# Kernel tuning notes

Measured on AMD Instinct MI355X. Metric: run time of the kernel, lower is better.

The kernel has to match this reference:

```python
import jax, jax.numpy as jnp
import numpy as np

P0 = 2   # tublet_size
P = 16   # patch_size
FC = 2   # flow channels (map_x, map_y)


def patchify(x, p0, p1, p2):
    # x: (B, C, T, H, W) -> (B, (T/p0)(H/p1)(W/p2), p0*p1*p2*C)
    B, C, T, H, W = x.shape
    x = x.reshape(B, C, T // p0, p0, H // p1, p1, W // p2, p2)
    x = x.transpose(0, 2, 4, 6, 3, 5, 7, 1)  # b t h w p0 p1 p2 c
    return x.reshape(B, (T // p0) * (H // p1) * (W // p2), p0 * p1 * p2 * C)


def unpatchify(x, p0, p1, p2, C, T, H, W):
    # x: (B, N, p0*p1*p2*C) -> (B, C, T, H, W)
    B = x.shape[0]
    x = x.reshape(B, T // p0, H // p1, W // p2, p0, p1, p2, C)
    x = x.transpose(0, 7, 1, 4, 2, 5, 3, 6)  # b c t p0 h p1 w p2
    return x.reshape(B, C, T, H, W)


def bilinear_warp(imgs, mx, my):
    # imgs: (B, C, T, H, W); mx, my: (B, T, H, W) absolute sample coords.
    # Equivalent of cv2.remap INTER_LINEAR with constant (zero) border.
    B, C, T, H, W = imgs.shape
    x0 = jnp.floor(mx)
    y0 = jnp.floor(my)
    wx = (mx - x0).reshape(B, 1, T, H * W)
    wy = (my - y0).reshape(B, 1, T, H * W)
    x0i = x0.astype(jnp.int32)
    y0i = y0.astype(jnp.int32)
    imgs_flat = imgs.reshape(B, C, T, H * W)

    def gather(yi, xi):
        yc = jnp.clip(yi, 0, H - 1)
        xc = jnp.clip(xi, 0, W - 1)
        idx = (yc * W + xc).reshape(B, 1, T, H * W)
        v = jnp.take_along_axis(imgs_flat, jnp.broadcast_to(idx, (B, C, T, H * W)), axis=-1)
        valid = ((yi >= 0) & (yi <= H - 1) & (xi >= 0) & (xi <= W - 1)).reshape(B, 1, T, H * W)
        return v * valid.astype(v.dtype)

    v00 = gather(y0i, x0i)
    v01 = gather(y0i, x0i + 1)
    v10 = gather(y0i + 1, x0i)
    v11 = gather(y0i + 1, x0i + 1)
    out = (v00 * (1 - wx) * (1 - wy) + v01 * wx * (1 - wy)
           + v10 * (1 - wx) * wy + v11 * wx * wy)
    return out.reshape(B, C, T, H, W)


def setup_inputs() -> dict:
    key = jax.random.key(0)
    k1, k2, k3 = jax.random.split(key, 3)
    B, C, T, H, W = 8, 3, 16, 224, 224
    N = (T // P0) * (H // P) * (W // P)         # 1568 tokens
    D = P0 * P * P * FC                         # 1024 per-token flow dim
    output = jax.random.normal(k1, (B, N, D), dtype=jnp.float32)
    raw_target = jax.random.normal(k2, (B, C, T, H, W), dtype=jnp.float32)
    mask = jax.random.randint(k3, (B, N), 0, 2) > 0
    return {"output": output, "raw_target": raw_target, "mask": mask}


def reference(output, raw_target, mask):
    B, C, T, H, W = raw_target.shape
    # tokens -> dense flow field (B, 2, T, H, W)
    flows = unpatchify(output, P0, P, P, FC, T, H, W)
    gx = jnp.arange(W, dtype=flows.dtype)               # (W,)
    gy = jnp.arange(H, dtype=flows.dtype)[:, None]      # (H, 1)
    mx = flows[:, 0] + gx                                # (B, T, H, W)
    my = flows[:, 1] + gy
    recons = bilinear_warp(raw_target, mx, my)           # (B, C, T, H, W)
    rec_p = patchify(recons, P0, P, P)                   # (B, N, p0*p1*p2*C)
    tgt_p = patchify(raw_target, P0, P, P)
    m = mask.astype(rec_p.dtype)[..., None]              # (B, N, 1)
    diff2 = (rec_p - tgt_p) ** 2 * m
    denom = jnp.maximum(m.sum(), 1.0) * rec_p.shape[-1]
    return diff2.sum() / denom
```

## Files before the change

### kernel.cpp

```cpp
#include <hip/hip_runtime.h>

#define Bd 8
#define Cd 3
#define Td 16
#define Hd 224
#define Wd 224
#define Nd 1568
#define HWd (Hd*Wd)
#define NPH 14
#define NPW 14
#define NT2 8
#define NSTRIP (Bd*NT2*NPH)
#define NUNIT (NSTRIP*2)
#define GRID_MAIN (NUNIT*3)
#define UPX (NUNIT/8)
#define HALO 2
#define SROWS (16 + 2*HALO)
#define LROW Wd
#define LDS_FLOATS (SROWS*LROW)
#define STG_GRAN (SROWS*56)
#define PATCH_ELEMS 1536.0

typedef const float __attribute__((address_space(1))) gfloat;
typedef float __attribute__((address_space(3))) sfloat;

__global__ __launch_bounds__(256, 8)
void flow_mse_strip(const float* __restrict__ outp,
                    const float* __restrict__ raw,
                    const int* __restrict__ mask,
                    float* __restrict__ partial,
                    int* __restrict__ scnt) {
    __shared__ float lds[LDS_FLOATS];
    __shared__ float sred[4];

    const int tid  = threadIdx.x;
    const int bid  = blockIdx.x;
    const int xcd  = bid & 7;
    const int slot = bid >> 3;
    const int c    = slot % 3;
    const int ul   = slot / 3;
    const int u    = xcd * UPX + ul;
    const int strip = u >> 1;
    const int i0    = u & 1;
    const int b     = strip / (NT2 * NPH);
    const int sr    = strip - b * (NT2 * NPH);
    const int t2    = sr / NPH;
    const int ph    = sr - t2 * NPH;
    const int t     = (t2 << 1) | i0;
    const int ybase = (ph << 4) - HALO;

    const float* plane = raw + ((size_t)(b * Cd + c) * Td + t) * HWd;
    #pragma unroll
    for (int it = 0; it < 5; ++it) {
        int v = tid + (it << 8);
        if (v < STG_GRAN) {
            int j    = v / 56;
            int col4 = v - j * 56;
            int yc   = min(max(ybase + j, 0), Hd - 1);
            const float* g = plane + yc * Wd + (col4 << 2);
            __builtin_amdgcn_global_load_lds((gfloat*)g, (sfloat*)(lds + (v << 2)),
                                             16, 0, 0);
        }
    }

    const int nbase = t2 * 196 + ph * NPW;
    const int lane  = tid & 63;
    bool mm = false;
    if (lane < NPW) mm = (mask[b * Nd + nbase + lane] != 0);
    const unsigned mw0   = (unsigned)(__ballot(mm) & 0x3FFFull);
    const int      tkcnt = __popc(mw0);

    __syncthreads();

    float acc = 0.f;
    const int py = tid >> 4, px = tid & 15;
    const int h  = (ph << 4) + py;
    const int bt = (py + HALO) * LROW;

    unsigned mw = mw0;
    while (mw) {
        const int pw = __ffs((int)mw) - 1;
        mw &= mw - 1;

        const float* fpf = outp + (((size_t)(b * Nd + nbase + pw)) << 10) + (i0 << 9);
        float2 f = ((const float2*)fpf)[tid];

        const int w = (pw << 4) + px;
        float mx = f.x + (float)w;
        float my = f.y + (float)h;
        float x0 = floorf(mx), y0 = floorf(my);
        float wx = mx - x0,    wy = my - y0;
        int x0i = (int)x0, y0i = (int)y0;
        int x1i = x0i + 1,  y1i = y0i + 1;

        bool vx0 = (x0i >= 0) && (x0i < Wd);
        bool vx1 = (x1i >= 0) && (x1i < Wd);
        bool vy0 = (y0i >= 0) && (y0i < Hd);
        bool vy1 = (y1i >= 0) && (y1i < Hd);

        float W00 = (1.f - wx) * (1.f - wy) * ((vx0 && vy0) ? 1.f : 0.f);
        float W01 = wx         * (1.f - wy) * ((vx1 && vy0) ? 1.f : 0.f);
        float W10 = (1.f - wx) * wy         * ((vx0 && vy1) ? 1.f : 0.f);
        float W11 = wx         * wy         * ((vx1 && vy1) ? 1.f : 0.f);

        int xc0 = min(max(x0i, 0), Wd - 1);
        int xc1 = min(max(x1i, 0), Wd - 1);
        int yc0 = min(max(y0i, 0), Hd - 1);
        int yc1 = min(max(y1i, 0), Hd - 1);
        int ly0 = yc0 - ybase, ly1 = yc1 - ybase;

        float tg = lds[bt + w];
        float rec;
        if ((ly0 >= 0) & (ly1 < SROWS)) {
            rec = lds[ly0 * LROW + xc0] * W00 + lds[ly0 * LROW + xc1] * W01
                + lds[ly1 * LROW + xc0] * W10 + lds[ly1 * LROW + xc1] * W11;
        } else {
            rec = plane[yc0 * Wd + xc0] * W00 + plane[yc0 * Wd + xc1] * W01
                + plane[yc1 * Wd + xc0] * W10 + plane[yc1 * Wd + xc1] * W11;
        }
        float d = rec - tg;
        acc += d * d;
    }

    for (int off = 32; off > 0; off >>= 1) acc += __shfl_down(acc, off, 64);
    if ((tid & 63) == 0) sred[tid >> 6] = acc;
    __syncthreads();
    if (tid == 0) {
        partial[bid] = sred[0] + sred[1] + sred[2] + sred[3];
        if (c == 0 && i0 == 0) scnt[strip] = tkcnt;
    }
}

__global__ void finalize_kernel(const float* __restrict__ partial,
                                const int* __restrict__ scnt,
                                float* __restrict__ out) {
    const int tid = threadIdx.x;
    double s = 0.0;
    for (int i = tid; i < GRID_MAIN; i += 256) s += (double)partial[i];
    int c = 0;
    for (int i = tid; i < NSTRIP; i += 256) c += scnt[i];
    for (int off = 32; off > 0; off >>= 1) {
        s += __shfl_down(s, off, 64);
        c += __shfl_down(c, off, 64);
    }
    __shared__ double sd[4];
    __shared__ int    sc[4];
    int lane = tid & 63, wid = tid >> 6;
    if (lane == 0) { sd[wid] = s; sc[wid] = c; }
    __syncthreads();
    if (tid == 0) {
        double st = sd[0] + sd[1] + sd[2] + sd[3];
        int    ct = sc[0] + sc[1] + sc[2] + sc[3];
        double denom = (double)(ct > 0 ? ct : 1) * PATCH_ELEMS;
        out[0] = (float)(st / denom);
    }
}

extern "C" void kernel_launch(void* const* d_in, const int* in_sizes, int n_in,
                              void* d_out, int out_size, void* d_ws, size_t ws_size,
                              hipStream_t stream) {
    const float* outp = (const float*)d_in[0];
    const float* raw  = (const float*)d_in[1];
    const int*   mask = (const int*)d_in[2];
    float* out = (float*)d_out;

    float* partial = (float*)d_ws;
    int*   scnt    = (int*)((char*)d_ws + GRID_MAIN * 4);

    flow_mse_strip<<<GRID_MAIN, 256, 0, stream>>>(outp, raw, mask, partial, scnt);
    finalize_kernel<<<1, 256, 0, stream>>>(partial, scnt, out);
}
```

Measured before the change: 160.3 us.

## Replace LDS strip staging with per-token direct global gather kernel

The kernel drops the per-strip LDS staging of image rows (with halo) and instead launches one block per token and frame, which exits early if the token is masked off. Each block gathers the bilinear taps and the target pixel straight from global memory for all three channels, so the flow is loaded once for all channels instead of once per channel block. The aim is to avoid staging rows that masked tokens never use and to drop the LDS fill and barrier. The cost is that neighbouring tokens no longer share staged data, so the design relies on the cache. The final kernel now counts the mask directly, and the grid grows to about 25k mostly short blocks.

```diff
diff --git a/kernel.cpp b/kernel.cpp
--- a/kernel.cpp
+++ b/kernel.cpp
@@ -7,138 +7,93 @@
 #define Wd 224
 #define Nd 1568
 #define HWd (Hd*Wd)
-#define NPH 14
-#define NPW 14
-#define NT2 8
-#define NSTRIP (Bd*NT2*NPH)
-#define NUNIT (NSTRIP*2)
-#define GRID_MAIN (NUNIT*3)
-#define UPX (NUNIT/8)
-#define HALO 2
-#define SROWS (16 + 2*HALO)
-#define LROW Wd
-#define LDS_FLOATS (SROWS*LROW)
-#define STG_GRAN (SROWS*56)
+#define NTOK (Bd*Nd)
+#define GRID_MAIN (NTOK*2)
 #define PATCH_ELEMS 1536.0
 
-typedef const float __attribute__((address_space(1))) gfloat;
-typedef float __attribute__((address_space(3))) sfloat;
+__global__ __launch_bounds__(256, 8)
+void flow_mse_gather(const float* __restrict__ outp,
+                     const float* __restrict__ raw,
+                     const int* __restrict__ mask,
+                     float* __restrict__ partial) {
+    const int tid = threadIdx.x;
+    const int bid = blockIdx.x;
+    const int ft  = bid >> 1;
+    const int i0  = bid & 1;
 
-__global__ __launch_bounds__(256, 8)
-void flow_mse_strip(const float* __restrict__ outp,
-                    const float* __restrict__ raw,
-                    const int* __restrict__ mask,
-                    float* __restrict__ partial,
-                    int* __restrict__ scnt) {
-    __shared__ float lds[LDS_FLOATS];
-    __shared__ float sred[4];
-
-    const int tid  = threadIdx.x;
-    const int bid  = blockIdx.x;
-    const int xcd  = bid & 7;
-    const int slot = bid >> 3;
-    const int c    = slot % 3;
-    const int ul   = slot / 3;
-    const int u    = xcd * UPX + ul;
-    const int strip = u >> 1;
-    const int i0    = u & 1;
-    const int b     = strip / (NT2 * NPH);
-    const int sr    = strip - b * (NT2 * NPH);
-    const int t2    = sr / NPH;
-    const int ph    = sr - t2 * NPH;
-    const int t     = (t2 << 1) | i0;
-    const int ybase = (ph << 4) - HALO;
-
-    const float* plane = raw + ((size_t)(b * Cd + c) * Td + t) * HWd;
-    #pragma unroll
-    for (int it = 0; it < 5; ++it) {
-        int v = tid + (it << 8);
-        if (v < STG_GRAN) {
-            int j    = v / 56;
-            int col4 = v - j * 56;
-            int yc   = min(max(ybase + j, 0), Hd - 1);
-            const float* g = plane + yc * Wd + (col4 << 2);
-            __builtin_amdgcn_global_load_lds((gfloat*)g, (sfloat*)(lds + (v << 2)),
-                                             16, 0, 0);
-        }
+    if (mask[ft] == 0) {
+        if (tid == 0) partial[bid] = 0.f;
+        return;
     }
 
-    const int nbase = t2 * 196 + ph * NPW;
-    const int lane  = tid & 63;
-    bool mm = false;
-    if (lane < NPW) mm = (mask[b * Nd + nbase + lane] != 0);
-    const unsigned mw0   = (unsigned)(__ballot(mm) & 0x3FFFull);
-    const int      tkcnt = __popc(mw0);
+    const int b  = ft / Nd;
+    const int n  = ft - b * Nd;
+    const int t2 = n / 196;
+    const int rm = n - t2 * 196;
+    const int ph = rm / 14;
+    const int pw = rm - ph * 14;
+    const int t  = (t2 << 1) | i0;
 
-    __syncthreads();
-
-    float acc = 0.f;
     const int py = tid >> 4, px = tid & 15;
     const int h  = (ph << 4) + py;
-    const int bt = (py + HALO) * LROW;
+    const int w  = (pw << 4) + px;
 
-    unsigned mw = mw0;
-    while (mw) {
-        const int pw = __ffs((int)mw) - 1;
-        mw &= mw - 1;
+    const float2 f = ((const float2*)(outp + ((size_t)ft << 10) + (i0 << 9)))[tid];
 
-        const float* fpf = outp + (((size_t)(b * Nd + nbase + pw)) << 10) + (i0 << 9);
-        float2 f = ((const float2*)fpf)[tid];
+    const float mx = f.x + (float)w;
+    const float my = f.y + (float)h;
+    const float x0 = floorf(mx), y0 = floorf(my);
+    const float wx = mx - x0,    wy = my - y0;
+    const int x0i = (int)x0, y0i = (int)y0;
+    const int x1i = x0i + 1,  y1i = y0i + 1;
 
-        const int w = (pw << 4) + px;
-        float mx = f.x + (float)w;
-        float my = f.y + (float)h;
-        float x0 = floorf(mx), y0 = floorf(my);
-        float wx = mx - x0,    wy = my - y0;
-        int x0i = (int)x0, y0i = (int)y0;
-        int x1i = x0i + 1,  y1i = y0i + 1;
+    const bool vx0 = (x0i >= 0) && (x0i < Wd);
+    const bool vx1 = (x1i >= 0) && (x1i < Wd);
+    const bool vy0 = (y0i >= 0) && (y0i < Hd);
+    const bool vy1 = (y1i >= 0) && (y1i < Hd);
 
-        bool vx0 = (x0i >= 0) && (x0i < Wd);
-        bool vx1 = (x1i >= 0) && (x1i < Wd);
-        bool vy0 = (y0i >= 0) && (y0i < Hd);
-        bool vy1 = (y1i >= 0) && (y1i < Hd);
+    const float W00 = (1.f - wx) * (1.f - wy) * ((vx0 && vy0) ? 1.f : 0.f);
+    const float W01 = wx         * (1.f - wy) * ((vx1 && vy0) ? 1.f : 0.f);
+    const float W10 = (1.f - wx) * wy         * ((vx0 && vy1) ? 1.f : 0.f);
+    const float W11 = wx         * wy         * ((vx1 && vy1) ? 1.f : 0.f);
 
-        float W00 = (1.f - wx) * (1.f - wy) * ((vx0 && vy0) ? 1.f : 0.f);
-        float W01 = wx         * (1.f - wy) * ((vx1 && vy0) ? 1.f : 0.f);
-        float W10 = (1.f - wx) * wy         * ((vx0 && vy1) ? 1.f : 0.f);
-        float W11 = wx         * wy         * ((vx1 && vy1) ? 1.f : 0.f);
+    const int xc0 = min(max(x0i, 0), Wd - 1);
+    const int xc1 = min(max(x1i, 0), Wd - 1);
+    const int yc0 = min(max(y0i, 0), Hd - 1);
+    const int yc1 = min(max(y1i, 0), Hd - 1);
 
-        int xc0 = min(max(x0i, 0), Wd - 1);
-        int xc1 = min(max(x1i, 0), Wd - 1);
-        int yc0 = min(max(y0i, 0), Hd - 1);
-        int yc1 = min(max(y1i, 0), Hd - 1);
-        int ly0 = yc0 - ybase, ly1 = yc1 - ybase;
+    const int i00 = yc0 * Wd + xc0;
+    const int i01 = yc0 * Wd + xc1;
+    const int i10 = yc1 * Wd + xc0;
+    const int i11 = yc1 * Wd + xc1;
+    const int itg = h * Wd + w;
 
-        float tg = lds[bt + w];
-        float rec;
-        if ((ly0 >= 0) & (ly1 < SROWS)) {
-            rec = lds[ly0 * LROW + xc0] * W00 + lds[ly0 * LROW + xc1] * W01
-                + lds[ly1 * LROW + xc0] * W10 + lds[ly1 * LROW + xc1] * W11;
-        } else {
-            rec = plane[yc0 * Wd + xc0] * W00 + plane[yc0 * Wd + xc1] * W01
-                + plane[yc1 * Wd + xc0] * W10 + plane[yc1 * Wd + xc1] * W11;
-        }
-        float d = rec - tg;
+    const float* base = raw + (size_t)(b * (Cd * Td) + t) * HWd;
+    float acc = 0.f;
+    #pragma unroll
+    for (int c = 0; c < Cd; ++c) {
+        const float* img = base + (size_t)c * (Td * HWd);
+        float rec = img[i00] * W00 + img[i01] * W01
+                  + img[i10] * W10 + img[i11] * W11;
+        float d = rec - img[itg];
         acc += d * d;
     }
 
+    __shared__ float sred[4];
     for (int off = 32; off > 0; off >>= 1) acc += __shfl_down(acc, off, 64);
     if ((tid & 63) == 0) sred[tid >> 6] = acc;
     __syncthreads();
-    if (tid == 0) {
-        partial[bid] = sred[0] + sred[1] + sred[2] + sred[3];
-        if (c == 0 && i0 == 0) scnt[strip] = tkcnt;
-    }
+    if (tid == 0) partial[bid] = sred[0] + sred[1] + sred[2] + sred[3];
 }
 
 __global__ void finalize_kernel(const float* __restrict__ partial,
-                                const int* __restrict__ scnt,
+                                const int* __restrict__ mask,
                                 float* __restrict__ out) {
     const int tid = threadIdx.x;
     double s = 0.0;
     for (int i = tid; i < GRID_MAIN; i += 256) s += (double)partial[i];
     int c = 0;
-    for (int i = tid; i < NSTRIP; i += 256) c += scnt[i];
+    for (int i = tid; i < NTOK; i += 256) c += (mask[i] != 0) ? 1 : 0;
     for (int off = 32; off > 0; off >>= 1) {
         s += __shfl_down(s, off, 64);
         c += __shfl_down(c, off, 64);
@@ -165,8 +120,7 @@
     float* out = (float*)d_out;
 
     float* partial = (float*)d_ws;
-    int*   scnt    = (int*)((char*)d_ws + GRID_MAIN * 4);
 
-    flow_mse_strip<<<GRID_MAIN, 256, 0, stream>>>(outp, raw, mask, partial, scnt);
-    finalize_kernel<<<1, 256, 0, stream>>>(partial, scnt, out);
+    flow_mse_gather<<<GRID_MAIN, 256, 0, stream>>>(outp, raw, mask, partial);
+    finalize_kernel<<<1, 256, 0, stream>>>(partial, mask, out);
 }
```

Measured after the change: 190.5 us. +18.8%, slower.
